# Kernel optimization log

Measured on AMD Instinct MI355X. Metric: run time of the kernel, lower is better.

The kernel has to match this reference:

```python
import jax, jax.numpy as jnp
import numpy as np

N = 262144        # number of 3D coordinate points (64^3 grid, flattened)
LW = 64           # layer_width
NOISE_DIM = 16
C_DIM = 3
NODES = 12        # 1 input node + 11 hidden graph nodes

# Frozen random-graph topology: predecessors of hidden node i (node 0 is the input node).
PREDS = ((0,), (1,), (2, 0), (3, 1, 0), (4, 2), (5, 3), (6, 4), (7, 5, 0), (8, 6), (9, 7), (10, 8))

def gauss(t):
    return jnp.exp(-0.5 * t * t)

# 'basic' activation set, cycled through graph nodes
ACTS = (jnp.tanh, jax.nn.elu, jax.nn.softplus, jnp.sin, gauss, jax.nn.sigmoid)


def setup_inputs() -> dict:
    key = jax.random.key(0)
    ks = jax.random.split(key, 16)
    n_g = NODES - 1
    inp = {
        "x": jax.random.normal(ks[0], (N, 1), jnp.float32),
        "y": jax.random.normal(ks[1], (N, 1), jnp.float32),
        "z": jax.random.normal(ks[2], (N, 1), jnp.float32),
        "r": jax.random.normal(ks[3], (N, 1), jnp.float32),
        "noise": jax.random.normal(ks[4], (N, NOISE_DIM), jnp.float32),
        # learned parameters
        "W_noise": jax.random.normal(ks[5], (NOISE_DIM, LW), jnp.float32) / np.sqrt(NOISE_DIM),
        "b_noise": jnp.zeros((LW,), jnp.float32),
        "W_x": jax.random.normal(ks[6], (1, LW), jnp.float32),
        "W_y": jax.random.normal(ks[7], (1, LW), jnp.float32),
        "W_z": jax.random.normal(ks[8], (1, LW), jnp.float32),
        "W_r": jax.random.normal(ks[9], (1, LW), jnp.float32),
        "W1": jax.random.normal(ks[10], (LW, LW), jnp.float32) / np.sqrt(LW),
        "b1": jnp.zeros((LW,), jnp.float32),
        "Wg": jax.random.normal(ks[11], (n_g, LW, LW), jnp.float32) / np.sqrt(LW),
        "bg": jnp.zeros((n_g, LW), jnp.float32),
        "W_out": jax.random.normal(ks[12], (LW, C_DIM), jnp.float32) / np.sqrt(LW),
        "b_out": jnp.zeros((C_DIM,), jnp.float32),
    }
    return inp


def reference(x, y, z, r, noise, W_noise, b_noise, W_x, W_y, W_z, W_r, W1, b1, Wg, bg, W_out, b_out):
    # input branches: tiny dim-1 linears + distinct pointwise activations
    noise_ = jnp.tanh(noise @ W_noise + b_noise)   # [N, LW]
    z_ = jax.nn.elu(z @ W_z)
    r_ = jax.nn.softplus(r @ W_r)
    y_ = jnp.tanh(y @ W_y)
    x_ = gauss(x @ W_x)
    f = jnp.sin(z_ + x_ + y_ + r_ + noise_)
    f = jnp.tanh(f @ W1 + b1)
    # randomly-wired graph of small linear+activation nodes (frozen topology)
    h = [f]
    for i, preds in enumerate(PREDS):
        s = h[preds[0]]
        for p in preds[1:]:
            s = s + h[p]
        h.append(ACTS[i % len(ACTS)](s @ Wg[i] + bg[i]))
    out = h[-1] @ W_out + b_out                    # combine node -> c_dim
    return jax.nn.sigmoid(out)                     # act_out (clip_loss=False)
```

## Files before the change

### kernel.cpp

```cpp
#include <hip/hip_runtime.h>

#define WRS 65

typedef _Float16 f16;
typedef f16  f16x4 __attribute__((ext_vector_type(4)));
typedef f16  f16x8 __attribute__((ext_vector_type(8)));
typedef __fp16 h16x2 __attribute__((ext_vector_type(2)));
typedef float f32x4  __attribute__((ext_vector_type(4)));
typedef float f32x16 __attribute__((ext_vector_type(16)));
typedef unsigned int u32;
typedef u32 u32x2 __attribute__((ext_vector_type(2)));
typedef u32 u32x4 __attribute__((ext_vector_type(4)));

#define LOG2E   1.4426950408889634f
#define LN2     0.6931471805599453f
#define C_TANH  2.8853900817779268f
#define C_SIN   0.15915494309189535f
#define C_SIG  -1.4426950408889634f
#define C_GAU  -0.7213475204444817f

__device__ __constant__ float NSCL[12] = {
    C_TANH, C_TANH, 1.0f, 1.0f, C_SIN, 1.0f, C_SIG, C_TANH, 1.0f, 1.0f, C_SIN, 1.0f
};

__device__ __forceinline__ float frcp(float x){ return __builtin_amdgcn_rcpf(x); }
__device__ __forceinline__ float fexp2(float x){ return __builtin_amdgcn_exp2f(x); }
__device__ __forceinline__ float flog2(float x){ return __builtin_amdgcn_logf(x); }
__device__ __forceinline__ float fsin1(float x){ return __builtin_amdgcn_sinf(x); }

template<int A> __device__ __forceinline__ float act(float v){
    if constexpr (A == 0){
        float t = fexp2(v);
        return 1.0f - 2.0f * frcp(1.0f + t);
    } else if constexpr (A == 1){
        float e = fexp2(v * LOG2E) - 1.0f;
        return v > 0.0f ? v : e;
    } else if constexpr (A == 2){
        float p = fexp2(-LOG2E * fabsf(v));
        return fmaxf(v, 0.0f) + LN2 * flog2(1.0f + p);
    } else if constexpr (A == 3){
        return fsin1(v);
    } else if constexpr (A == 4){
        return fexp2(v * v * C_GAU);
    } else {
        return frcp(1.0f + fexp2(v));
    }
}

__device__ __forceinline__ f16x4 pack4(float a, float b, float c, float d){
    u32x2 u;
    u[0] = __builtin_bit_cast(u32, __builtin_amdgcn_cvt_pkrtz(a, b));
    u[1] = __builtin_bit_cast(u32, __builtin_amdgcn_cvt_pkrtz(c, d));
    return __builtin_bit_cast(f16x4, u);
}
__device__ __forceinline__ f16x8 cat8(f16x4 lo, f16x4 hi){
    u32x2 a = __builtin_bit_cast(u32x2, lo), b = __builtin_bit_cast(u32x2, hi);
    u32x4 u; u[0] = a[0]; u[1] = a[1]; u[2] = b[0]; u[3] = b[1];
    return __builtin_bit_cast(f16x8, u);
}

#define MFMA32(a, b, c) __builtin_amdgcn_mfma_f32_32x32x16_f16((a), (b), (c), 0, 0, 0)

template<int ACTI>
__device__ __forceinline__ void node32(const f16* __restrict__ wr,
                                       const float* __restrict__ bs,
                                       const int hf4,
                                       const f16x8 B[4], f16x8 OUT[4])
{
    f16x4 pk[2][4];
    #pragma unroll
    for (int t = 0; t < 2; ++t){
        f32x16 ac;
        #pragma unroll
        for (int g = 0; g < 4; ++g){
            f32x4 bv = *(const f32x4*)(bs + 32 * t + 8 * g + hf4);
            ac[4*g+0] = bv[0]; ac[4*g+1] = bv[1]; ac[4*g+2] = bv[2]; ac[4*g+3] = bv[3];
        }
        #pragma unroll
        for (int kc = 0; kc < 4; ++kc)
            ac = MFMA32(*(const f16x8*)(wr + t * 2048 + kc * 512), B[kc], ac);
        #pragma unroll
        for (int g = 0; g < 4; ++g)
            pk[t][g] = pack4(act<ACTI>(ac[4*g+0]), act<ACTI>(ac[4*g+1]),
                             act<ACTI>(ac[4*g+2]), act<ACTI>(ac[4*g+3]));
    }
    #pragma unroll
    for (int kc = 0; kc < 4; ++kc) OUT[kc] = cat8(pk[0][kc], pk[1][kc]);
}

__global__ __launch_bounds__(1024, 1) void inr_mfma7_kernel(
    const float* __restrict__ gx, const float* __restrict__ gy,
    const float* __restrict__ gz, const float* __restrict__ gr,
    const float* __restrict__ gnoise,
    const float* __restrict__ W_noise, const float* __restrict__ b_noise,
    const float* __restrict__ W_x, const float* __restrict__ W_y,
    const float* __restrict__ W_z, const float* __restrict__ W_r,
    const float* __restrict__ W1, const float* __restrict__ b1,
    const float* __restrict__ Wg, const float* __restrict__ bg,
    const float* __restrict__ W_out, const float* __restrict__ b_out,
    float* __restrict__ out, int nt, int niter)
{
    __shared__ __align__(16) f16   wfrag[12][2][4][64][8];
    __shared__ __align__(16) f16   nfrag[2][64][8];
    __shared__ __align__(16) f16   ofrag[4][64][8];
    __shared__ __align__(16) float b_s[12][64];
    __shared__ __align__(16) float wvs[4][64];
    __shared__ __align__(16) float bns[64];
    __shared__            float bout_s[4];
    __shared__ __align__(16) float wstage[64 * WRS];

    const int tid  = threadIdx.x;
    const int lane = tid & 63;
    const int n2   = lane & 31;
    const int hf   = lane >> 5;
    const int hf4  = 4 * hf;

    if (tid < 768){
        int node = tid >> 6, f = tid & 63;
        b_s[node][f] = NSCL[node] * ((node == 0) ? b1[f] : bg[(node - 1) * 64 + f]);
    }
    if (tid < 256){
        int vec = tid >> 6, f = tid & 63;
        float v;
        if      (vec == 0){ float w = W_x[f]; v = C_GAU * w * w; }
        else if (vec == 1){ v = C_TANH * W_y[f]; }
        else if (vec == 2){ v = W_z[f]; }
        else              { v = W_r[f]; }
        wvs[vec][f] = v;
    }
    if (tid < 64) bns[tid] = C_TANH * b_noise[tid];
    if (tid < 4)  bout_s[tid] = (tid < 3) ? C_SIG * b_out[tid] : 0.0f;
    if (tid < 128){
        int t = tid >> 6, ln = tid & 63, m = ln & 31, h = ln >> 5;
        f16x8 v;
        #pragma unroll
        for (int j = 0; j < 8; ++j) v[j] = (f16)(C_TANH * W_noise[(8 * h + j) * 64 + 32 * t + m]);
        *(f16x8*)&nfrag[t][ln][0] = v;
    }
    if (tid < 256){
        int kc = tid >> 6, ln = tid & 63, m = ln & 31, h = ln >> 5;
        f16x8 v;
        #pragma unroll
        for (int j = 0; j < 8; ++j){
            int kf = 8 * kc + 32 * (j >> 2) + 4 * h + (j & 3);
            v[j] = (m < 3) ? (f16)(C_SIG * W_out[kf * 3 + m]) : (f16)0.0f;
        }
        *(f16x8*)&ofrag[kc][ln][0] = v;
    }
    for (int node = 0; node < 12; ++node){
        const float* Wsrc = (node == 0) ? W1 : (Wg + (node - 1) * 4096);
        const float  scl  = NSCL[node];
        __syncthreads();
        {
            float4 v = ((const float4*)Wsrc)[tid];
            int row = tid >> 4, col = (tid & 15) * 4;
            float* d = wstage + row * WRS + col;
            d[0] = v.x; d[1] = v.y; d[2] = v.z; d[3] = v.w;
        }
        __syncthreads();
        if (tid < 512){
            int t = tid >> 8, kc = (tid >> 6) & 3, ln = tid & 63, m = ln & 31, h = ln >> 5;
            f16x8 v;
            #pragma unroll
            for (int j = 0; j < 8; ++j){
                int kf = 8 * kc + 32 * (j >> 2) + 4 * h + (j & 3);
                v[j] = (f16)(scl * wstage[kf * WRS + 32 * t + m]);
            }
            *(f16x8*)&wfrag[node][t][kc][ln][0] = v;
        }
    }
    __syncthreads();

    #define WPTR(NI) (&wfrag[NI][0][0][lane][0])
    #define N1(NI, ACTI, A, OUT)  node32<ACTI>(WPTR(NI), &b_s[NI][0], hf4, A, OUT)
    #define N2(NI, ACTI, A, B, OUT) do {                                            \
        f16x8 s_[4];                                                                \
        _Pragma("unroll")                                                           \
        for (int kc_ = 0; kc_ < 4; ++kc_) s_[kc_] = A[kc_] + B[kc_];                \
        node32<ACTI>(WPTR(NI), &b_s[NI][0], hf4, s_, OUT);                          \
    } while (0)
    #define N3(NI, ACTI, A, B, C, OUT) do {                                         \
        f16x8 s_[4];                                                                \
        _Pragma("unroll")                                                           \
        for (int kc_ = 0; kc_ < 4; ++kc_) s_[kc_] = A[kc_] + B[kc_] + C[kc_];       \
        node32<ACTI>(WPTR(NI), &b_s[NI][0], hf4, s_, OUT);                          \
    } while (0)

    const int wvid = tid >> 6;

    for (int it = 0; it < niter; ++it){
        const int tile = (it * gridDim.x + blockIdx.x) * 16 + wvid;
        if (tile >= nt) break;
        const int myp = tile * 32 + n2;

        const float xs = gx[myp], ys = gy[myp], zs = gz[myp], rs = gr[myp];
        const float xs2 = xs * xs;
        f16x8 nb;
        {
            const float4 a4 = *(const float4*)(gnoise + (size_t)myp * 16 + 8 * hf);
            const float4 b4 = *(const float4*)(gnoise + (size_t)myp * 16 + 8 * hf + 4);
            nb = cat8(pack4(a4.x, a4.y, a4.z, a4.w), pack4(b4.x, b4.y, b4.z, b4.w));
        }
        f16x8 sg[4];
        {
            f16x4 pkg[2][4];
            #pragma unroll
            for (int t = 0; t < 2; ++t){
                f32x16 ac;
                #pragma unroll
                for (int i = 0; i < 16; ++i) ac[i] = 0.0f;
                ac = MFMA32(*(const f16x8*)&nfrag[t][lane][0], nb, ac);
                #pragma unroll
                for (int g = 0; g < 4; ++g){
                    const int fb = 32 * t + 8 * g + hf4;
                    const f32x4 wx2 = *(const f32x4*)&wvs[0][fb];
                    const f32x4 wyt = *(const f32x4*)&wvs[1][fb];
                    const f32x4 wz  = *(const f32x4*)&wvs[2][fb];
                    const f32x4 wr_ = *(const f32x4*)&wvs[3][fb];
                    const f32x4 bn  = *(const f32x4*)&bns[fb];
                    float gv[4];
                    #pragma unroll
                    for (int r = 0; r < 4; ++r){
                        float az = zs * wz[r];
                        float ez = fexp2(az * LOG2E) - 1.0f;
                        float velu = az > 0.0f ? az : ez;
                        float vga = fexp2(xs2 * wx2[r]);
                        float ty = fexp2(ys * wyt[r]);
                        float vty = 1.0f - 2.0f * frcp(1.0f + ty);
                        float ar = rs * wr_[r];
                        float vsp = fmaxf(ar, 0.0f) + LN2 * flog2(1.0f + fexp2(-LOG2E * fabsf(ar)));
                        float tp = fexp2(ac[4 * g + r] + bn[r]);
                        float vtp = 1.0f - 2.0f * frcp(1.0f + tp);
                        float v = velu + vga + vty + vsp + vtp;
                        gv[r] = fsin1(v * C_SIN);
                    }
                    pkg[t][g] = pack4(gv[0], gv[1], gv[2], gv[3]);
                }
            }
            #pragma unroll
            for (int kc = 0; kc < 4; ++kc) sg[kc] = cat8(pkg[0][kc], pkg[1][kc]);
        }

        f16x8 h0[4], r0[4], r1[4], r2[4], r3[4];
        N1(0,  0, sg, h0);
        N1(1,  0, h0, r0);
        N1(2,  1, r0, r1);
        N2(3,  2, r1, h0, r2);
        N3(4,  3, r2, r0, h0, r3);
        N2(5,  4, r3, r1, r0);
        N2(6,  5, r0, r2, r1);
        N2(7,  0, r1, r3, r2);
        N3(8,  1, r2, r0, h0, r3);
        N2(9,  2, r3, r1, r0);
        N2(10, 3, r0, r2, r1);
        N2(11, 4, r1, r3, r2);

        {
            f32x16 om;
            #pragma unroll
            for (int i = 0; i < 16; ++i) om[i] = 0.0f;
            #pragma unroll
            for (int kc = 0; kc < 4; ++kc)
                om = MFMA32(*(const f16x8*)&ofrag[kc][lane][0], r2[kc], om);
            if (hf == 0){
                #pragma unroll
                for (int r = 0; r < 3; ++r)
                    out[(size_t)myp * 3 + r] = frcp(1.0f + fexp2(om[r] + bout_s[r]));
            }
        }
    }
    #undef N1
    #undef N2
    #undef N3
    #undef WPTR
}

extern "C" void kernel_launch(void* const* d_in, const int* in_sizes, int n_in,
                              void* d_out, int out_size, void* d_ws, size_t ws_size,
                              hipStream_t stream)
{
    const float* x       = (const float*)d_in[0];
    const float* y       = (const float*)d_in[1];
    const float* z       = (const float*)d_in[2];
    const float* r       = (const float*)d_in[3];
    const float* noise   = (const float*)d_in[4];
    const float* W_noise = (const float*)d_in[5];
    const float* b_noise = (const float*)d_in[6];
    const float* W_x     = (const float*)d_in[7];
    const float* W_y     = (const float*)d_in[8];
    const float* W_z     = (const float*)d_in[9];
    const float* W_r     = (const float*)d_in[10];
    const float* W1      = (const float*)d_in[11];
    const float* b1      = (const float*)d_in[12];
    const float* Wg      = (const float*)d_in[13];
    const float* bg      = (const float*)d_in[14];
    const float* W_out   = (const float*)d_in[15];
    const float* b_out   = (const float*)d_in[16];
    float* out = (float*)d_out;

    const int n     = in_sizes[0];
    const int nt    = n / 32;
    const int grid  = 256;
    const int tiles_per_pass = grid * 16;
    const int niter = (nt + tiles_per_pass - 1) / tiles_per_pass;
    inr_mfma7_kernel<<<dim3(grid), dim3(1024), 0, stream>>>(
        x, y, z, r, noise, W_noise, b_noise, W_x, W_y, W_z, W_r,
        W1, b1, Wg, bg, W_out, b_out, out, nt, niter);
}
```

Before: 166.9 us.

## Process two point tiles per wave to reuse weight fragments and interleave MFMAs

```diff
diff --git a/kernel.cpp b/kernel.cpp
--- a/kernel.cpp
+++ b/kernel.cpp
@@ -1,6 +1,4 @@
 #include <hip/hip_runtime.h>
-
-#define WRS 65
 
 typedef _Float16 f16;
 typedef f16  f16x4 __attribute__((ext_vector_type(4)));
@@ -61,34 +59,48 @@
 
 #define MFMA32(a, b, c) __builtin_amdgcn_mfma_f32_32x32x16_f16((a), (b), (c), 0, 0, 0)
 
-template<int ACTI>
-__device__ __forceinline__ void node32(const f16* __restrict__ wr,
-                                       const float* __restrict__ bs,
-                                       const int hf4,
-                                       const f16x8 B[4], f16x8 OUT[4])
+template<int ACTI, int NP>
+__device__ __forceinline__ void node32x2(const f16* __restrict__ wr,
+                                         const float* __restrict__ bs,
+                                         const int hf4,
+                                         const f16x8 A0[2][4], const f16x8 A1[2][4], const f16x8 A2[2][4],
+                                         f16x8 OUT[2][4])
 {
-    f16x4 pk[2][4];
+    f16x4 pkP[2][4], pkQ[2][4];
     #pragma unroll
     for (int t = 0; t < 2; ++t){
-        f32x16 ac;
+        f32x16 aP, aQ;
         #pragma unroll
         for (int g = 0; g < 4; ++g){
             f32x4 bv = *(const f32x4*)(bs + 32 * t + 8 * g + hf4);
-            ac[4*g+0] = bv[0]; ac[4*g+1] = bv[1]; ac[4*g+2] = bv[2]; ac[4*g+3] = bv[3];
-        }
-        #pragma unroll
-        for (int kc = 0; kc < 4; ++kc)
-            ac = MFMA32(*(const f16x8*)(wr + t * 2048 + kc * 512), B[kc], ac);
-        #pragma unroll
-        for (int g = 0; g < 4; ++g)
-            pk[t][g] = pack4(act<ACTI>(ac[4*g+0]), act<ACTI>(ac[4*g+1]),
-                             act<ACTI>(ac[4*g+2]), act<ACTI>(ac[4*g+3]));
+            aP[4*g+0] = bv[0]; aP[4*g+1] = bv[1]; aP[4*g+2] = bv[2]; aP[4*g+3] = bv[3];
+            aQ[4*g+0] = bv[0]; aQ[4*g+1] = bv[1]; aQ[4*g+2] = bv[2]; aQ[4*g+3] = bv[3];
+        }
+        #pragma unroll
+        for (int kc = 0; kc < 4; ++kc){
+            f16x8 Af = *(const f16x8*)(wr + t * 2048 + kc * 512);
+            f16x8 bP = A0[0][kc], bQ = A0[1][kc];
+            if constexpr (NP >= 2){ bP = bP + A1[0][kc]; bQ = bQ + A1[1][kc]; }
+            if constexpr (NP >= 3){ bP = bP + A2[0][kc]; bQ = bQ + A2[1][kc]; }
+            aP = MFMA32(Af, bP, aP);
+            aQ = MFMA32(Af, bQ, aQ);
+        }
+        #pragma unroll
+        for (int g = 0; g < 4; ++g){
+            pkP[t][g] = pack4(act<ACTI>(aP[4*g+0]), act<ACTI>(aP[4*g+1]),
+                              act<ACTI>(aP[4*g+2]), act<ACTI>(aP[4*g+3]));
+            pkQ[t][g] = pack4(act<ACTI>(aQ[4*g+0]), act<ACTI>(aQ[4*g+1]),
+                              act<ACTI>(aQ[4*g+2]), act<ACTI>(aQ[4*g+3]));
+        }
     }
     #pragma unroll
-    for (int kc = 0; kc < 4; ++kc) OUT[kc] = cat8(pk[0][kc], pk[1][kc]);
-}
-
-__global__ __launch_bounds__(1024, 1) void inr_mfma7_kernel(
+    for (int kc = 0; kc < 4; ++kc){
+        OUT[0][kc] = cat8(pkP[0][kc], pkP[1][kc]);
+        OUT[1][kc] = cat8(pkQ[0][kc], pkQ[1][kc]);
+    }
+}
+
+__global__ __launch_bounds__(512, 2) void inr_mfma8_kernel(
     const float* __restrict__ gx, const float* __restrict__ gy,
     const float* __restrict__ gz, const float* __restrict__ gr,
     const float* __restrict__ gnoise,
@@ -107,7 +119,6 @@
     __shared__ __align__(16) float wvs[4][64];
     __shared__ __align__(16) float bns[64];
     __shared__            float bout_s[4];
-    __shared__ __align__(16) float wstage[64 * WRS];
 
     const int tid  = threadIdx.x;
     const int lane = tid & 63;
@@ -115,8 +126,8 @@
     const int hf   = lane >> 5;
     const int hf4  = 4 * hf;
 
-    if (tid < 768){
-        int node = tid >> 6, f = tid & 63;
+    for (int i = tid; i < 768; i += 512){
+        int node = i >> 6, f = i & 63;
         b_s[node][f] = NSCL[node] * ((node == 0) ? b1[f] : bg[(node - 1) * 64 + f]);
     }
     if (tid < 256){
@@ -147,62 +158,49 @@
         }
         *(f16x8*)&ofrag[kc][ln][0] = v;
     }
-    for (int node = 0; node < 12; ++node){
-        const float* Wsrc = (node == 0) ? W1 : (Wg + (node - 1) * 4096);
-        const float  scl  = NSCL[node];
-        __syncthreads();
-        {
-            float4 v = ((const float4*)Wsrc)[tid];
-            int row = tid >> 4, col = (tid & 15) * 4;
-            float* d = wstage + row * WRS + col;
-            d[0] = v.x; d[1] = v.y; d[2] = v.z; d[3] = v.w;
-        }
-        __syncthreads();
-        if (tid < 512){
-            int t = tid >> 8, kc = (tid >> 6) & 3, ln = tid & 63, m = ln & 31, h = ln >> 5;
+    {
+        const int t = tid >> 8, kc = (tid >> 6) & 3, ln = tid & 63, m = ln & 31, h = ln >> 5;
+        int kfo[8];
+        #pragma unroll
+        for (int j = 0; j < 8; ++j)
+            kfo[j] = (8 * kc + 32 * (j >> 2) + 4 * h + (j & 3)) * 64 + 32 * t + m;
+        #pragma unroll
+        for (int node = 0; node < 12; ++node){
+            const float* Wsrc = (node == 0) ? W1 : (Wg + (node - 1) * 4096);
+            const float  scl  = NSCL[node];
             f16x8 v;
             #pragma unroll
-            for (int j = 0; j < 8; ++j){
-                int kf = 8 * kc + 32 * (j >> 2) + 4 * h + (j & 3);
-                v[j] = (f16)(scl * wstage[kf * WRS + 32 * t + m]);
+            for (int j = 0; j < 8; ++j) v[j] = (f16)(scl * Wsrc[kfo[j]]);
+            *(f16x8*)&wfrag[node][t][kc][ln][0] = v;
+        }
+    }
+    __syncthreads();
+
+    #define WPTR(NI) (&wfrag[NI][0][0][lane][0])
+    #define N1(NI, ACTI, A, OUT)        node32x2<ACTI,1>(WPTR(NI), &b_s[NI][0], hf4, A, A, A, OUT)
+    #define N2(NI, ACTI, A, B, OUT)     node32x2<ACTI,2>(WPTR(NI), &b_s[NI][0], hf4, A, B, B, OUT)
+    #define N3(NI, ACTI, A, B, C, OUT)  node32x2<ACTI,3>(WPTR(NI), &b_s[NI][0], hf4, A, B, C, OUT)
+
+    const int wvid = tid >> 6;
+
+    for (int it = 0; it < niter; ++it){
+        const int tbase = ((it * gridDim.x + blockIdx.x) * 8 + wvid) * 2;
+        if (tbase >= nt) break;
+
+        f16x8 sg[2][4];
+        int myp2[2];
+        #pragma unroll
+        for (int tt = 0; tt < 2; ++tt){
+            const int myp = (tbase + tt) * 32 + n2;
+            myp2[tt] = myp;
+            const float xs = gx[myp], ys = gy[myp], zs = gz[myp], rs = gr[myp];
+            const float xs2 = xs * xs;
+            f16x8 nb;
+            {
+                const float4 a4 = *(const float4*)(gnoise + (size_t)myp * 16 + 8 * hf);
+                const float4 b4 = *(const float4*)(gnoise + (size_t)myp * 16 + 8 * hf + 4);
+                nb = cat8(pack4(a4.x, a4.y, a4.z, a4.w), pack4(b4.x, b4.y, b4.z, b4.w));
             }
-            *(f16x8*)&wfrag[node][t][kc][ln][0] = v;
-        }
-    }
-    __syncthreads();
-
-    #define WPTR(NI) (&wfrag[NI][0][0][lane][0])
-    #define N1(NI, ACTI, A, OUT)  node32<ACTI>(WPTR(NI), &b_s[NI][0], hf4, A, OUT)
-    #define N2(NI, ACTI, A, B, OUT) do {                                            \
-        f16x8 s_[4];                                                                \
-        _Pragma("unroll")                                                           \
-        for (int kc_ = 0; kc_ < 4; ++kc_) s_[kc_] = A[kc_] + B[kc_];                \
-        node32<ACTI>(WPTR(NI), &b_s[NI][0], hf4, s_, OUT);                          \
-    } while (0)
-    #define N3(NI, ACTI, A, B, C, OUT) do {                                         \
-        f16x8 s_[4];                                                                \
-        _Pragma("unroll")                                                           \
-        for (int kc_ = 0; kc_ < 4; ++kc_) s_[kc_] = A[kc_] + B[kc_] + C[kc_];       \
-        node32<ACTI>(WPTR(NI), &b_s[NI][0], hf4, s_, OUT);                          \
-    } while (0)
-
-    const int wvid = tid >> 6;
-
-    for (int it = 0; it < niter; ++it){
-        const int tile = (it * gridDim.x + blockIdx.x) * 16 + wvid;
-        if (tile >= nt) break;
-        const int myp = tile * 32 + n2;
-
-        const float xs = gx[myp], ys = gy[myp], zs = gz[myp], rs = gr[myp];
-        const float xs2 = xs * xs;
-        f16x8 nb;
-        {
-            const float4 a4 = *(const float4*)(gnoise + (size_t)myp * 16 + 8 * hf);
-            const float4 b4 = *(const float4*)(gnoise + (size_t)myp * 16 + 8 * hf + 4);
-            nb = cat8(pack4(a4.x, a4.y, a4.z, a4.w), pack4(b4.x, b4.y, b4.z, b4.w));
-        }
-        f16x8 sg[4];
-        {
             f16x4 pkg[2][4];
             #pragma unroll
             for (int t = 0; t < 2; ++t){
@@ -222,26 +220,22 @@
                     #pragma unroll
                     for (int r = 0; r < 4; ++r){
                         float az = zs * wz[r];
-                        float ez = fexp2(az * LOG2E) - 1.0f;
-                        float velu = az > 0.0f ? az : ez;
+                        float velu = az > 0.0f ? az : (fexp2(az * LOG2E) - 1.0f);
                         float vga = fexp2(xs2 * wx2[r]);
-                        float ty = fexp2(ys * wyt[r]);
-                        float vty = 1.0f - 2.0f * frcp(1.0f + ty);
+                        float vty = 1.0f - 2.0f * frcp(1.0f + fexp2(ys * wyt[r]));
                         float ar = rs * wr_[r];
                         float vsp = fmaxf(ar, 0.0f) + LN2 * flog2(1.0f + fexp2(-LOG2E * fabsf(ar)));
-                        float tp = fexp2(ac[4 * g + r] + bn[r]);
-                        float vtp = 1.0f - 2.0f * frcp(1.0f + tp);
-                        float v = velu + vga + vty + vsp + vtp;
-                        gv[r] = fsin1(v * C_SIN);
+                        float vtp = 1.0f - 2.0f * frcp(1.0f + fexp2(ac[4 * g + r] + bn[r]));
+                        gv[r] = fsin1((velu + vga + vty + vsp + vtp) * C_SIN);
                     }
                     pkg[t][g] = pack4(gv[0], gv[1], gv[2], gv[3]);
                 }
             }
             #pragma unroll
-            for (int kc = 0; kc < 4; ++kc) sg[kc] = cat8(pkg[0][kc], pkg[1][kc]);
-        }
-
-        f16x8 h0[4], r0[4], r1[4], r2[4], r3[4];
+            for (int kc = 0; kc < 4; ++kc) sg[tt][kc] = cat8(pkg[0][kc], pkg[1][kc]);
+        }
+
+        f16x8 h0[2][4], r0[2][4], r1[2][4], r2[2][4], r3[2][4];
         N1(0,  0, sg, h0);
         N1(1,  0, h0, r0);
         N1(2,  1, r0, r1);
@@ -255,17 +249,18 @@
         N2(10, 3, r0, r2, r1);
         N2(11, 4, r1, r3, r2);
 
-        {
+        #pragma unroll
+        for (int tt = 0; tt < 2; ++tt){
             f32x16 om;
             #pragma unroll
             for (int i = 0; i < 16; ++i) om[i] = 0.0f;
             #pragma unroll
             for (int kc = 0; kc < 4; ++kc)
-                om = MFMA32(*(const f16x8*)&ofrag[kc][lane][0], r2[kc], om);
+                om = MFMA32(*(const f16x8*)&ofrag[kc][lane][0], r2[tt][kc], om);
             if (hf == 0){
                 #pragma unroll
                 for (int r = 0; r < 3; ++r)
-                    out[(size_t)myp * 3 + r] = frcp(1.0f + fexp2(om[r] + bout_s[r]));
+                    out[(size_t)myp2[tt] * 3 + r] = frcp(1.0f + fexp2(om[r] + bout_s[r]));
             }
         }
     }
@@ -301,9 +296,9 @@
     const int n     = in_sizes[0];
     const int nt    = n / 32;
     const int grid  = 256;
-    const int tiles_per_pass = grid * 16;
+    const int tiles_per_pass = grid * 8 * 2;
     const int niter = (nt + tiles_per_pass - 1) / tiles_per_pass;
-    inr_mfma7_kernel<<<dim3(grid), dim3(1024), 0, stream>>>(
+    inr_mfma8_kernel<<<dim3(grid), dim3(512), 0, stream>>>(
         x, y, z, r, noise, W_noise, b_noise, W_x, W_y, W_z, W_r,
         W1, b1, Wg, bg, W_out, b_out, out, nt, niter);
 }
```

Result: faster. 160.7 us, median of 2 (-3.7%).
